# Kernel tuning notes

Hardware: AMD Instinct MI355X
Metric: run time of the kernel (lower is better)

The kernel has to match this reference:

```python
import jax, jax.numpy as jnp
import numpy as np

B, HID, REC, NC, T = 512, 196, 488, 35, 120
BN_EPS = 1e-3


def _bn(x, g, b):
    # eval-mode CustomBatchNorm1d: running_mean=0, running_var=1
    return g * (x / jnp.sqrt(1.0 + BN_EPS)) + b


def _gru(x, Wih, Whh, bih, bhh):
    """Standard torch nn.GRU (batch_first), h0 = 0. x: [B,T,D] -> [B,T,H]."""
    H = Whh.shape[1]
    def step(h, xt):
        xg = xt @ Wih.T + bih          # [B,3H]
        hg = h @ Whh.T + bhh           # [B,3H]
        xr, xz, xn = jnp.split(xg, 3, axis=1)
        hr, hz, hn = jnp.split(hg, 3, axis=1)
        r = jax.nn.sigmoid(xr + hr)
        z = jax.nn.sigmoid(xz + hz)
        n = jnp.tanh(xn + r * hn)
        h2 = (1.0 - z) * n + z * h
        return h2, h2
    h0 = jnp.zeros((x.shape[0], H), x.dtype)
    _, ys = jax.lax.scan(step, h0, jnp.swapaxes(x, 0, 1))
    return jnp.swapaxes(ys, 0, 1)


def _custom_gru(x, Wih, Whh, bih):
    """CustomGRUCell (eval mode: prev_target=0 so weight_tf term vanishes)."""
    H = Whh.shape[1]
    Whh_rz = Whh[:2 * H]
    Whh_n = Whh[2 * H:]
    b_r, b_z, b_n = bih[:H], bih[H:2 * H], bih[2 * H:]
    def step(h, xt):
        xg = xt @ Wih.T                 # [B,3H], no bias in F.linear
        xr, xz, xn = jnp.split(xg, 3, axis=1)
        hg = h @ Whh_rz.T               # only r,z rows needed (h_h chunk unused)
        hr, hz = jnp.split(hg, 2, axis=1)
        r = jax.nn.sigmoid(xr + hr + b_r)
        u = jax.nn.sigmoid(xz + hz + b_z)
        n = jax.nn.softmax(xn + (r * h) @ Whh_n.T + b_n, axis=1)
        h2 = (1.0 - u) * n + u * h
        return h2, h2
    h0 = jnp.zeros((x.shape[0], H), x.dtype)
    _, ys = jax.lax.scan(step, h0, jnp.swapaxes(x, 0, 1))
    return jnp.swapaxes(ys, 0, 1)


def setup_inputs() -> dict:
    key = jax.random.key(0)
    ks = jax.random.split(key, 16)
    s = 0.05
    inp = {
        "z_in": jax.random.normal(ks[0], (B, HID), jnp.float32),
        "W0": jax.random.normal(ks[1], (HID, HID), jnp.float32) * s,
        "b0": jnp.zeros((HID,), jnp.float32),
        "g0": jnp.full((1, HID), 0.1, jnp.float32),
        "beta0": jnp.zeros((1, HID), jnp.float32),
        "W1": jax.random.normal(ks[2], (HID, HID), jnp.float32) * s,
        "b1": jnp.zeros((HID,), jnp.float32),
        "g1": jnp.full((1, HID), 0.1, jnp.float32),
        "beta1": jnp.zeros((1, HID), jnp.float32),
        "gru0_Wih": jax.random.normal(ks[3], (3 * REC, HID), jnp.float32) * s,
        "gru0_Whh": jax.random.normal(ks[4], (3 * REC, REC), jnp.float32) * s,
        "gru0_bih": jax.random.normal(ks[5], (3 * REC,), jnp.float32) * s,
        "gru0_bhh": jax.random.normal(ks[6], (3 * REC,), jnp.float32) * s,
        "gru1_Wih": jax.random.normal(ks[7], (3 * REC, REC), jnp.float32) * s,
        "gru1_Whh": jax.random.normal(ks[8], (3 * REC, REC), jnp.float32) * s,
        "gru1_bih": jax.random.normal(ks[9], (3 * REC,), jnp.float32) * s,
        "gru1_bhh": jax.random.normal(ks[10], (3 * REC,), jnp.float32) * s,
        "cell_Wih": jax.random.normal(ks[11], (3 * NC, REC), jnp.float32) * s,
        "cell_Whh": jax.random.normal(ks[12], (3 * NC, NC), jnp.float32) * s,
        "cell_bih": jax.random.normal(ks[13], (3 * NC,), jnp.float32) * s,
    }
    return inp


def reference(z_in, W0, b0, g0, beta0, W1, b1, g1, beta1,
              gru0_Wih, gru0_Whh, gru0_bih, gru0_bhh,
              gru1_Wih, gru1_Whh, gru1_bih, gru1_bhh,
              cell_Wih, cell_Whh, cell_bih):
    z = _bn(z_in @ W0.T + b0, g0, beta0)
    z = _bn(z @ W1.T + b1, g1, beta1)
    z_reps = jnp.broadcast_to(z[:, None, :], (z.shape[0], T, z.shape[1]))
    x = _gru(z_reps, gru0_Wih, gru0_Whh, gru0_bih, gru0_bhh)
    x = _gru(x, gru1_Wih, gru1_Whh, gru1_bih, gru1_bhh)
    x_out = _custom_gru(x, cell_Wih, cell_Whh, cell_bih)  # [B,T,NCHARS]
    return x_out
```

## Files before the change

### kernel.cpp

```cpp
#include <hip/hip_runtime.h>
#include <math.h>

#define Bsz 512
#define HID 196
#define REC 488
#define NC  35
#define TT  120
#define G3  1464
#define NSLOT 123

#define KT   8
#define NCH  61
#define NB   61
#define CELLB 32
#define NGRID (3*NB + CELLB)
#define WSL  (NCH*KT*24)

struct CellSmem { float xs[16][492]; float hs[16][36]; float rh[16][36]; };

__device__ __forceinline__ float sigmoidf_(float x) { return 1.0f / (1.0f + __expf(-x)); }

__device__ __forceinline__ void gbar(int* bar, int target) {
  __syncthreads();
  if (threadIdx.x == 0) {
    __builtin_amdgcn_fence(__ATOMIC_RELEASE, "agent");
    __hip_atomic_fetch_add(bar, 1, __ATOMIC_RELAXED, __HIP_MEMORY_SCOPE_AGENT);
    while (__hip_atomic_load(bar, __ATOMIC_RELAXED, __HIP_MEMORY_SCOPE_AGENT) < target)
      __builtin_amdgcn_s_sleep(2);
    __builtin_amdgcn_fence(__ATOMIC_ACQUIRE, "agent");
  }
  __syncthreads();
}

__global__ void dense_bn_kernel(const float* __restrict__ X, const float* __restrict__ W,
                                const float* __restrict__ bias, const float* __restrict__ g,
                                const float* __restrict__ beta, float* __restrict__ Y) {
  __shared__ float xs[HID];
  int b = blockIdx.x;
  for (int k = threadIdx.x; k < HID; k += blockDim.x) xs[k] = X[(size_t)b*HID + k];
  __syncthreads();
  int j = threadIdx.x;
  if (j < HID) {
    const float4* wr = (const float4*)(W + (size_t)j*HID);
    float acc = 0.f;
    #pragma unroll 7
    for (int k4 = 0; k4 < HID/4; ++k4) {
      float4 w4 = wr[k4];
      acc += xs[4*k4+0]*w4.x + xs[4*k4+1]*w4.y + xs[4*k4+2]*w4.z + xs[4*k4+3]*w4.w;
    }
    float v = (acc + bias[j]) * 0.9995003746f;
    Y[(size_t)b*HID + j] = g[j]*v + beta[j];
  }
}

__global__ __launch_bounds__(256)
void xg0v2_kernel(const float* __restrict__ Z, const float* __restrict__ Wih,
                  const float* __restrict__ bih, float* __restrict__ XGT) {
  __shared__ float zs[HID*4];
  int b0 = blockIdx.x << 2;
  for (int idx = threadIdx.x; idx < HID*4; idx += 256) {
    int k = idx >> 2, i = idx & 3;
    zs[idx] = Z[(size_t)(b0+i)*HID + k];
  }
  __syncthreads();
  for (int c = threadIdx.x; c < G3; c += 256) {
    const float4* wr = (const float4*)(Wih + (size_t)c*HID);
    float a0=0.f,a1=0.f,a2=0.f,a3=0.f;
    for (int k4 = 0; k4 < HID/4; ++k4) {
      float4 w = wr[k4];
      const float* zp = zs + (k4<<4);
      a0=fmaf(w.x,zp[0],a0);  a1=fmaf(w.x,zp[1],a1);  a2=fmaf(w.x,zp[2],a2);  a3=fmaf(w.x,zp[3],a3);
      a0=fmaf(w.y,zp[4],a0);  a1=fmaf(w.y,zp[5],a1);  a2=fmaf(w.y,zp[6],a2);  a3=fmaf(w.y,zp[7],a3);
      a0=fmaf(w.z,zp[8],a0);  a1=fmaf(w.z,zp[9],a1);  a2=fmaf(w.z,zp[10],a2); a3=fmaf(w.z,zp[11],a3);
      a0=fmaf(w.w,zp[12],a0); a1=fmaf(w.w,zp[13],a1); a2=fmaf(w.w,zp[14],a2); a3=fmaf(w.w,zp[15],a3);
    }
    float bb = bih[c];
    XGT[(size_t)c*Bsz + b0+0] = a0 + bb;
    XGT[(size_t)c*Bsz + b0+1] = a1 + bb;
    XGT[(size_t)c*Bsz + b0+2] = a2 + bb;
    XGT[(size_t)c*Bsz + b0+3] = a3 + bb;
  }
}

__global__ __launch_bounds__(256)
void wtrans_kernel(const float* __restrict__ Whh0, const float* __restrict__ Wih1,
                   const float* __restrict__ Whh1, float* __restrict__ Wt2) {
  int blk = blockIdx.x;
  int stage = blk / NB, j = blk - stage*NB;
  const float* Wsrc = (stage==0) ? Whh0 : (stage==1) ? Wih1 : Whh1;
  float* dst = Wt2 + (size_t)blk*WSL;
  for (int idx = threadIdx.x; idx < WSL; idx += 256) {
    int ck = idx / 192, rem = idx - ck*192;
    int k = rem / 24, r = rem - k*24;
    int g = r >> 3, cl = r & 7;
    dst[idx] = Wsrc[(size_t)(g*REC + j*8 + cl)*REC + ck*8 + k];
  }
}

__device__ __forceinline__ void gemm24s(const float* __restrict__ AT, int b,
                                        const float* __restrict__ wp,
                                        float (&acc)[24])
{
  float av[KT], nv[KT];
  #pragma unroll
  for (int k = 0; k < KT; ++k) av[k] = AT[(size_t)k*Bsz + b];
  for (int ck = 0; ck < NCH; ++ck) {
    if (ck + 1 < NCH) {
      const float* src = AT + (size_t)(ck+1)*KT*Bsz + b;
      #pragma unroll
      for (int k = 0; k < KT; ++k) nv[k] = src[(size_t)k*Bsz];
    }
    const float* w = wp + ck*192;
    #pragma unroll
    for (int k = 0; k < KT; ++k) {
      float a = av[k];
      #pragma unroll
      for (int r = 0; r < 24; ++r)
        acc[r] = fmaf(a, w[k*24 + r], acc[r]);
    }
    #pragma unroll
    for (int k = 0; k < KT; ++k) av[k] = nv[k];
  }
}

__global__ __launch_bounds__(512)
void pers_kernel(const float* __restrict__ xg0T,
                 float* __restrict__ h0T, float* __restrict__ h1T,
                 float* __restrict__ xg1T, float* __restrict__ hc,
                 float* __restrict__ out,
                 const float* __restrict__ Wt2,
                 const float* __restrict__ bhh0,
                 const float* __restrict__ bih1, const float* __restrict__ bhh1,
                 const float* __restrict__ cWih, const float* __restrict__ cWhh,
                 const float* __restrict__ cb, int* __restrict__ bar)
{
  __shared__ CellSmem S;
  const int blk = blockIdx.x;
  const int tid = threadIdx.x;
  const int stage = (blk < NB) ? 0 : (blk < 2*NB) ? 1 : (blk < 3*NB) ? 2 : 3;
  const int l = tid & 63, w = tid >> 6;
  const float* wslice = Wt2 + (size_t)blk*WSL;

  for (int s = 0; s < NSLOT; ++s) {
    if (stage == 0) {
      if (s < TT) {
        int j = blk;
        const float* hprevT = h0T + (size_t)((s+1)&1)*REC*Bsz;
        float*       hnewT  = h0T + (size_t)(s&1)*REC*Bsz;
        float acc[24] = {0};
        gemm24s(hprevT, tid, wslice, acc);
        int b = tid, c0 = j*8;
        #pragma unroll
        for (int cl = 0; cl < 8; ++cl) {
          int c = c0 + cl;
          float xrv = xg0T[(size_t)c*Bsz + b];
          float xzv = xg0T[(size_t)(REC+c)*Bsz + b];
          float xnv = xg0T[(size_t)(2*REC+c)*Bsz + b];
          float r = sigmoidf_(xrv + acc[cl]      + bhh0[c]);
          float z = sigmoidf_(xzv + acc[8+cl]    + bhh0[REC+c]);
          float n = tanhf   (xnv + r*(acc[16+cl] + bhh0[2*REC+c]));
          hnewT[(size_t)c*Bsz + b] = (1.f-z)*n + z*hprevT[(size_t)c*Bsz + b];
        }
      }
    } else if (stage == 1) {
      if (s >= 1 && s <= TT) {
        int t1 = s - 1;
        const float* xT   = h0T  + (size_t)(t1&1)*REC*Bsz;
        float*       xgwT = xg1T + (size_t)(t1&1)*G3*Bsz;
        float acc[24] = {0};
        gemm24s(xT, tid, wslice, acc);
        int b = tid, c0 = (blk - NB)*8;
        #pragma unroll
        for (int cl = 0; cl < 8; ++cl) {
          int c = c0 + cl;
          xgwT[(size_t)c*Bsz + b]         = acc[cl];
          xgwT[(size_t)(REC+c)*Bsz + b]   = acc[8+cl];
          xgwT[(size_t)(2*REC+c)*Bsz + b] = acc[16+cl];
        }
      }
    } else if (stage == 2) {
      if (s >= 2 && s <= TT+1) {
        int t2 = s - 2;
        const float* hprevT = h1T  + (size_t)((t2+1)&1)*REC*Bsz;
        float*       hnewT  = h1T  + (size_t)(t2&1)*REC*Bsz;
        const float* xgrT   = xg1T + (size_t)(t2&1)*G3*Bsz;
        float acc[24] = {0};
        gemm24s(hprevT, tid, wslice, acc);
        int b = tid, c0 = (blk - 2*NB)*8;
        #pragma unroll
        for (int cl = 0; cl < 8; ++cl) {
          int c = c0 + cl;
          float xrv = xgrT[(size_t)c*Bsz + b];
          float xzv = xgrT[(size_t)(REC+c)*Bsz + b];
          float xnv = xgrT[(size_t)(2*REC+c)*Bsz + b];
          float r = sigmoidf_(xrv + acc[cl]   + bih1[c]     + bhh1[c]);
          float z = sigmoidf_(xzv + acc[8+cl] + bih1[REC+c] + bhh1[REC+c]);
          float n = tanhf   (xnv + bih1[2*REC+c] + r*(acc[16+cl] + bhh1[2*REC+c]));
          hnewT[(size_t)c*Bsz + b] = (1.f-z)*n + z*hprevT[(size_t)c*Bsz + b];
        }
      }
    } else {
      if (s >= 3) {
        int t3 = s - 3;
        int b0 = (blk - 3*NB) << 4;
        const float* xT = h1T + (size_t)(t3&1)*REC*Bsz;
        const float* hp = hc  + (size_t)((t3+1)&1)*Bsz*NC;
        float*       hn = hc  + (size_t)(t3&1)*Bsz*NC;
        for (int idx = tid; idx < 16*REC; idx += 512) {
          int k = idx >> 4, it = idx & 15;
          S.xs[it][k] = xT[(size_t)k*Bsz + b0 + it];
        }
        if (l < NC) {
          #pragma unroll
          for (int q = 0; q < 2; ++q) {
            int it = (w<<1) + q;
            S.hs[it][l] = hp[(size_t)(b0+it)*NC + l];
          }
        }
        __syncthreads();
        for (int q = 0; q < 2; ++q) {
          int it = (w<<1) + q;
          int b = b0 + it;
          float v = -1e30f, u = 0.f, hpc = 0.f;
          if (l < NC) {
            const float4* wr4 = (const float4*)(cWih + (size_t)l*REC);
            const float4* wz4 = (const float4*)(cWih + (size_t)(NC+l)*REC);
            const float4* wn4 = (const float4*)(cWih + (size_t)(2*NC+l)*REC);
            const float4* xs4 = (const float4*)(S.xs[it]);
            float xr=0.f, xz=0.f, xn=0.f;
            #pragma unroll 2
            for (int k4 = 0; k4 < REC/4; ++k4) {
              float4 xv = xs4[k4];
              float4 wa = wr4[k4], wb = wz4[k4], wc = wn4[k4];
              xr += wa.x*xv.x + wa.y*xv.y + wa.z*xv.z + wa.w*xv.w;
              xz += wb.x*xv.x + wb.y*xv.y + wb.z*xv.z + wb.w*xv.w;
              xn += wc.x*xv.x + wc.y*xv.y + wc.z*xv.z + wc.w*xv.w;
            }
            float hr=0.f, hz=0.f;
            for (int k = 0; k < NC; ++k) {
              float hv = S.hs[it][k];
              hr = fmaf(hv, cWhh[(size_t)l*NC + k], hr);
              hz = fmaf(hv, cWhh[(size_t)(NC+l)*NC + k], hz);
            }
            float r = sigmoidf_(xr + hr + cb[l]);
            u       = sigmoidf_(xz + hz + cb[NC+l]);
            hpc = S.hs[it][l];
            S.rh[it][l] = r * hpc;
            v = xn;
          }
          __syncthreads();
          if (l < NC) {
            float hnn = 0.f;
            for (int k = 0; k < NC; ++k)
              hnn = fmaf(S.rh[it][k], cWhh[(size_t)(2*NC+l)*NC + k], hnn);
            v = v + hnn + cb[2*NC+l];
          }
          float m = v;
          #pragma unroll
          for (int o = 32; o; o >>= 1) m = fmaxf(m, __shfl_xor(m, o));
          float e = (l < NC) ? __expf(v - m) : 0.f;
          float ss = e;
          #pragma unroll
          for (int o = 32; o; o >>= 1) ss += __shfl_xor(ss, o);
          if (l < NC) {
            float h2 = (1.f - u)*(e/ss) + u*hpc;
            hn[(size_t)b*NC + l] = h2;
            out[((size_t)b*TT + t3)*NC + l] = h2;
          }
          __syncthreads();
        }
      }
    }
    gbar(bar, NGRID*(s+1));
  }
}

extern "C" void kernel_launch(void* const* d_in, const int* in_sizes, int n_in,
                              void* d_out, int out_size, void* d_ws, size_t ws_size,
                              hipStream_t stream) {
  const float* z_in  = (const float*)d_in[0];
  const float* W0    = (const float*)d_in[1];
  const float* b0    = (const float*)d_in[2];
  const float* g0    = (const float*)d_in[3];
  const float* beta0 = (const float*)d_in[4];
  const float* W1    = (const float*)d_in[5];
  const float* b1    = (const float*)d_in[6];
  const float* g1    = (const float*)d_in[7];
  const float* beta1 = (const float*)d_in[8];
  const float* Wih0  = (const float*)d_in[9];
  const float* Whh0  = (const float*)d_in[10];
  const float* bih0  = (const float*)d_in[11];
  const float* bhh0  = (const float*)d_in[12];
  const float* Wih1  = (const float*)d_in[13];
  const float* Whh1  = (const float*)d_in[14];
  const float* bih1  = (const float*)d_in[15];
  const float* bhh1  = (const float*)d_in[16];
  const float* cWih  = (const float*)d_in[17];
  const float* cWhh  = (const float*)d_in[18];
  const float* cbih  = (const float*)d_in[19];
  float* out = (float*)d_out;

  float* ws   = (float*)d_ws;
  int*   bar  = (int*)ws;
  float* h0T  = ws   + 256;
  float* h1T  = h0T  + 2*(size_t)REC*Bsz;
  float* hcb  = h1T  + 2*(size_t)REC*Bsz;
  float* xg1T = hcb  + 2*(size_t)Bsz*NC;
  float* xg0T = xg1T + 2*(size_t)G3*Bsz;
  float* z1   = xg0T + (size_t)G3*Bsz;
  float* z2   = z1   + (size_t)Bsz*HID;
  float* Wt2  = z2   + (size_t)Bsz*HID;

  size_t zero_floats = 256 + 4*(size_t)REC*Bsz + 2*(size_t)Bsz*NC;
  hipMemsetAsync(ws, 0, zero_floats*sizeof(float), stream);

  dense_bn_kernel<<<Bsz, 256, 0, stream>>>(z_in, W0, b0, g0, beta0, z1);
  dense_bn_kernel<<<Bsz, 256, 0, stream>>>(z1,   W1, b1, g1, beta1, z2);
  xg0v2_kernel   <<<128, 256, 0, stream>>>(z2, Wih0, bih0, xg0T);
  wtrans_kernel  <<<3*NB, 256, 0, stream>>>(Whh0, Wih1, Whh1, Wt2);

  pers_kernel<<<NGRID, 512, 0, stream>>>(xg0T, h0T, h1T, xg1T, hcb, out,
                                         Wt2, bhh0, bih1, bhh1, cWih, cWhh, cbih, bar);
}
```

Before: 11.72 ms.

## Retile recurrent GEMM to 2 rows x 12 columns per thread with wave-uniform weights

Changes the per-thread work split in the persistent GRU GEMM. Each thread used to compute one batch row times 24 gate columns; now each computes two batch rows (float2 loads) times 12 columns, with waves split across row groups and column halves. The weight slice is re-laid out so each wave reads its own 12-column half, with a wave-uniform index via readfirstlane so those reads can become scalar loads. This aims to halve per-FMA weight traffic, vectorize activation loads and double-buffer both operands, at the cost of more registers.

```diff
diff --git a/kernel.cpp b/kernel.cpp
--- a/kernel.cpp
+++ b/kernel.cpp
@@ -9,12 +9,10 @@
 #define G3  1464
 #define NSLOT 123
 
-#define KT   8
-#define NCH  61
 #define NB   61
 #define CELLB 32
 #define NGRID (3*NB + CELLB)
-#define WSL  (NCH*KT*24)
+#define WSL  (REC*24)
 
 struct CellSmem { float xs[16][492]; float hs[16][36]; float rh[16][36]; };
 
@@ -84,42 +82,75 @@
 
 __global__ __launch_bounds__(256)
 void wtrans_kernel(const float* __restrict__ Whh0, const float* __restrict__ Wih1,
-                   const float* __restrict__ Whh1, float* __restrict__ Wt2) {
+                   const float* __restrict__ Whh1, float* __restrict__ Wt) {
   int blk = blockIdx.x;
   int stage = blk / NB, j = blk - stage*NB;
   const float* Wsrc = (stage==0) ? Whh0 : (stage==1) ? Wih1 : Whh1;
-  float* dst = Wt2 + (size_t)blk*WSL;
+  float* dst = Wt + (size_t)blk*WSL;
   for (int idx = threadIdx.x; idx < WSL; idx += 256) {
-    int ck = idx / 192, rem = idx - ck*192;
-    int k = rem / 24, r = rem - k*24;
-    int g = r >> 3, cl = r & 7;
-    dst[idx] = Wsrc[(size_t)(g*REC + j*8 + cl)*REC + ck*8 + k];
-  }
-}
-
-__device__ __forceinline__ void gemm24s(const float* __restrict__ AT, int b,
-                                        const float* __restrict__ wp,
-                                        float (&acc)[24])
+    int k = idx / 24, t = idx - k*24;
+    int cw = t / 12, u = t - cw*12;
+    int g = u >> 2, oc = u & 3;
+    dst[idx] = Wsrc[(size_t)(g*REC + j*8 + cw*4 + oc)*REC + k];
+  }
+}
+
+__device__ __forceinline__ void gemm2x12(const float* __restrict__ AT, int rbase,
+                                         const float* __restrict__ wp,
+                                         float (&acc)[24])
 {
-  float av[KT], nv[KT];
+  float2 A0[4], A1[4];
+  float  W0s[48], W1s[48];
+  const float* abase = AT + rbase;
   #pragma unroll
-  for (int k = 0; k < KT; ++k) av[k] = AT[(size_t)k*Bsz + b];
-  for (int ck = 0; ck < NCH; ++ck) {
-    if (ck + 1 < NCH) {
-      const float* src = AT + (size_t)(ck+1)*KT*Bsz + b;
-      #pragma unroll
-      for (int k = 0; k < KT; ++k) nv[k] = src[(size_t)k*Bsz];
-    }
-    const float* w = wp + ck*192;
+  for (int kk = 0; kk < 4; ++kk) A0[kk] = *(const float2*)(abase + (size_t)kk*Bsz);
+  #pragma unroll
+  for (int kk = 0; kk < 4; ++kk)
     #pragma unroll
-    for (int k = 0; k < KT; ++k) {
-      float a = av[k];
-      #pragma unroll
-      for (int r = 0; r < 24; ++r)
-        acc[r] = fmaf(a, w[k*24 + r], acc[r]);
+    for (int i = 0; i < 12; ++i) W0s[kk*12+i] = wp[kk*24 + i];
+
+  for (int ck = 0; ck < 122; ck += 2) {
+    int kb = ck*4;
+    {
+      const float* an = abase + (size_t)(kb+4)*Bsz;
+      const float* wn = wp + (size_t)(kb+4)*24;
+      #pragma unroll
+      for (int kk = 0; kk < 4; ++kk) A1[kk] = *(const float2*)(an + (size_t)kk*Bsz);
+      #pragma unroll
+      for (int kk = 0; kk < 4; ++kk)
+        #pragma unroll
+        for (int i = 0; i < 12; ++i) W1s[kk*12+i] = wn[kk*24 + i];
     }
     #pragma unroll
-    for (int k = 0; k < KT; ++k) av[k] = nv[k];
+    for (int kk = 0; kk < 4; ++kk) {
+      float x = A0[kk].x, y = A0[kk].y;
+      #pragma unroll
+      for (int i = 0; i < 12; ++i) {
+        float wv = W0s[kk*12+i];
+        acc[i*2+0] = fmaf(x, wv, acc[i*2+0]);
+        acc[i*2+1] = fmaf(y, wv, acc[i*2+1]);
+      }
+    }
+    if (ck + 2 < 122) {
+      const float* an = abase + (size_t)(kb+8)*Bsz;
+      const float* wn = wp + (size_t)(kb+8)*24;
+      #pragma unroll
+      for (int kk = 0; kk < 4; ++kk) A0[kk] = *(const float2*)(an + (size_t)kk*Bsz);
+      #pragma unroll
+      for (int kk = 0; kk < 4; ++kk)
+        #pragma unroll
+        for (int i = 0; i < 12; ++i) W0s[kk*12+i] = wn[kk*24 + i];
+    }
+    #pragma unroll
+    for (int kk = 0; kk < 4; ++kk) {
+      float x = A1[kk].x, y = A1[kk].y;
+      #pragma unroll
+      for (int i = 0; i < 12; ++i) {
+        float wv = W1s[kk*12+i];
+        acc[i*2+0] = fmaf(x, wv, acc[i*2+0]);
+        acc[i*2+1] = fmaf(y, wv, acc[i*2+1]);
+      }
+    }
   }
 }
 
@@ -128,7 +159,7 @@
                  float* __restrict__ h0T, float* __restrict__ h1T,
                  float* __restrict__ xg1T, float* __restrict__ hc,
                  float* __restrict__ out,
-                 const float* __restrict__ Wt2,
+                 const float* __restrict__ Wt,
                  const float* __restrict__ bhh0,
                  const float* __restrict__ bih1, const float* __restrict__ bhh1,
                  const float* __restrict__ cWih, const float* __restrict__ cWhh,
@@ -139,27 +170,38 @@
   const int tid = threadIdx.x;
   const int stage = (blk < NB) ? 0 : (blk < 2*NB) ? 1 : (blk < 3*NB) ? 2 : 3;
   const int l = tid & 63, w = tid >> 6;
-  const float* wslice = Wt2 + (size_t)blk*WSL;
+  const int w_u = __builtin_amdgcn_readfirstlane(w);
+  const int rw = w_u & 3, cw = w_u >> 2;
+  const int rbase = rw*128 + 2*l;
+  const float* wslice = Wt + (size_t)blk*WSL + cw*12;
+  const int jloc = blk - stage*NB;
+  const int co0 = jloc*8 + cw*4;
 
   for (int s = 0; s < NSLOT; ++s) {
     if (stage == 0) {
       if (s < TT) {
-        int j = blk;
         const float* hprevT = h0T + (size_t)((s+1)&1)*REC*Bsz;
         float*       hnewT  = h0T + (size_t)(s&1)*REC*Bsz;
         float acc[24] = {0};
-        gemm24s(hprevT, tid, wslice, acc);
-        int b = tid, c0 = j*8;
-        #pragma unroll
-        for (int cl = 0; cl < 8; ++cl) {
-          int c = c0 + cl;
-          float xrv = xg0T[(size_t)c*Bsz + b];
-          float xzv = xg0T[(size_t)(REC+c)*Bsz + b];
-          float xnv = xg0T[(size_t)(2*REC+c)*Bsz + b];
-          float r = sigmoidf_(xrv + acc[cl]      + bhh0[c]);
-          float z = sigmoidf_(xzv + acc[8+cl]    + bhh0[REC+c]);
-          float n = tanhf   (xnv + r*(acc[16+cl] + bhh0[2*REC+c]));
-          hnewT[(size_t)c*Bsz + b] = (1.f-z)*n + z*hprevT[(size_t)c*Bsz + b];
+        gemm2x12(hprevT, rbase, wslice, acc);
+        #pragma unroll
+        for (int oc = 0; oc < 4; ++oc) {
+          int c = co0 + oc;
+          float2 xr = *(const float2*)(xg0T + (size_t)c*Bsz + rbase);
+          float2 xz = *(const float2*)(xg0T + (size_t)(REC+c)*Bsz + rbase);
+          float2 xn = *(const float2*)(xg0T + (size_t)(2*REC+c)*Bsz + rbase);
+          float2 hp = *(const float2*)(hprevT + (size_t)c*Bsz + rbase);
+          float br = bhh0[c], bz = bhh0[REC+c], bn = bhh0[2*REC+c];
+          float r0 = sigmoidf_(xr.x + acc[oc*2]       + br);
+          float r1 = sigmoidf_(xr.y + acc[oc*2+1]     + br);
+          float z0 = sigmoidf_(xz.x + acc[(4+oc)*2]   + bz);
+          float z1 = sigmoidf_(xz.y + acc[(4+oc)*2+1] + bz);
+          float n0 = tanhf(xn.x + r0*(acc[(8+oc)*2]   + bn));
+          float n1 = tanhf(xn.y + r1*(acc[(8+oc)*2+1] + bn));
+          float2 o;
+          o.x = (1.f-z0)*n0 + z0*hp.x;
+          o.y = (1.f-z1)*n1 + z1*hp.y;
+          *(float2*)(hnewT + (size_t)c*Bsz + rbase) = o;
         }
       }
     } else if (stage == 1) {
@@ -168,14 +210,17 @@
         const float* xT   = h0T  + (size_t)(t1&1)*REC*Bsz;
         float*       xgwT = xg1T + (size_t)(t1&1)*G3*Bsz;
         float acc[24] = {0};
-        gemm24s(xT, tid, wslice, acc);
-        int b = tid, c0 = (blk - NB)*8;
-        #pragma unroll
-        for (int cl = 0; cl < 8; ++cl) {
-          int c = c0 + cl;
-          xgwT[(size_t)c*Bsz + b]         = acc[cl];
-          xgwT[(size_t)(REC+c)*Bsz + b]   = acc[8+cl];
-          xgwT[(size_t)(2*REC+c)*Bsz + b] = acc[16+cl];
+        gemm2x12(xT, rbase, wslice, acc);
+        #pragma unroll
+        for (int oc = 0; oc < 4; ++oc) {
+          int c = co0 + oc;
+          float2 vr, vz, vn;
+          vr.x = acc[oc*2];       vr.y = acc[oc*2+1];
+          vz.x = acc[(4+oc)*2];   vz.y = acc[(4+oc)*2+1];
+          vn.x = acc[(8+oc)*2];   vn.y = acc[(8+oc)*2+1];
+          *(float2*)(xgwT + (size_t)c*Bsz + rbase)         = vr;
+          *(float2*)(xgwT + (size_t)(REC+c)*Bsz + rbase)   = vz;
+          *(float2*)(xgwT + (size_t)(2*REC+c)*Bsz + rbase) = vn;
         }
       }
     } else if (stage == 2) {
@@ -185,18 +230,27 @@
         float*       hnewT  = h1T  + (size_t)(t2&1)*REC*Bsz;
         const float* xgrT   = xg1T + (size_t)(t2&1)*G3*Bsz;
         float acc[24] = {0};
-        gemm24s(hprevT, tid, wslice, acc);
-        int b = tid, c0 = (blk - 2*NB)*8;
-        #pragma unroll
-        for (int cl = 0; cl < 8; ++cl) {
-          int c = c0 + cl;
-          float xrv = xgrT[(size_t)c*Bsz + b];
-          float xzv = xgrT[(size_t)(REC+c)*Bsz + b];
-          float xnv = xgrT[(size_t)(2*REC+c)*Bsz + b];
-          float r = sigmoidf_(xrv + acc[cl]   + bih1[c]     + bhh1[c]);
-          float z = sigmoidf_(xzv + acc[8+cl] + bih1[REC+c] + bhh1[REC+c]);
-          float n = tanhf   (xnv + bih1[2*REC+c] + r*(acc[16+cl] + bhh1[2*REC+c]));
-          hnewT[(size_t)c*Bsz + b] = (1.f-z)*n + z*hprevT[(size_t)c*Bsz + b];
+        gemm2x12(hprevT, rbase, wslice, acc);
+        #pragma unroll
+        for (int oc = 0; oc < 4; ++oc) {
+          int c = co0 + oc;
+          float2 xr = *(const float2*)(xgrT + (size_t)c*Bsz + rbase);
+          float2 xz = *(const float2*)(xgrT + (size_t)(REC+c)*Bsz + rbase);
+          float2 xn = *(const float2*)(xgrT + (size_t)(2*REC+c)*Bsz + rbase);
+          float2 hp = *(const float2*)(hprevT + (size_t)c*Bsz + rbase);
+          float br = bih1[c] + bhh1[c];
+          float bz = bih1[REC+c] + bhh1[REC+c];
+          float bnx = bih1[2*REC+c], bnh = bhh1[2*REC+c];
+          float r0 = sigmoidf_(xr.x + acc[oc*2]       + br);
+          float r1 = sigmoidf_(xr.y + acc[oc*2+1]     + br);
+          float z0 = sigmoidf_(xz.x + acc[(4+oc)*2]   + bz);
+          float z1 = sigmoidf_(xz.y + acc[(4+oc)*2+1] + bz);
+          float n0 = tanhf(xn.x + bnx + r0*(acc[(8+oc)*2]   + bnh));
+          float n1 = tanhf(xn.y + bnx + r1*(acc[(8+oc)*2+1] + bnh));
+          float2 o;
+          o.x = (1.f-z0)*n0 + z0*hp.x;
+          o.y = (1.f-z1)*n1 + z1*hp.y;
+          *(float2*)(hnewT + (size_t)c*Bsz + rbase) = o;
         }
       }
     } else {
@@ -309,7 +363,7 @@
   float* xg0T = xg1T + 2*(size_t)G3*Bsz;
   float* z1   = xg0T + (size_t)G3*Bsz;
   float* z2   = z1   + (size_t)Bsz*HID;
-  float* Wt2  = z2   + (size_t)Bsz*HID;
+  float* Wt   = z2   + (size_t)Bsz*HID;
 
   size_t zero_floats = 256 + 4*(size_t)REC*Bsz + 2*(size_t)Bsz*NC;
   hipMemsetAsync(ws, 0, zero_floats*sizeof(float), stream);
@@ -317,8 +371,8 @@
   dense_bn_kernel<<<Bsz, 256, 0, stream>>>(z_in, W0, b0, g0, beta0, z1);
   dense_bn_kernel<<<Bsz, 256, 0, stream>>>(z1,   W1, b1, g1, beta1, z2);
   xg0v2_kernel   <<<128, 256, 0, stream>>>(z2, Wih0, bih0, xg0T);
-  wtrans_kernel  <<<3*NB, 256, 0, stream>>>(Whh0, Wih1, Whh1, Wt2);
+  wtrans_kernel  <<<3*NB, 256, 0, stream>>>(Whh0, Wih1, Whh1, Wt);
 
   pers_kernel<<<NGRID, 512, 0, stream>>>(xg0T, h0T, h1T, xg1T, hcb, out,
-                                         Wt2, bhh0, bih1, bhh1, cWih, cWhh, cbih, bar);
-}
+                                         Wt, bhh0, bih1, bhh1, cWih, cWhh, cbih, bar);
+}
```

Result: slower. 18.92 ms (+61.5%).
